# Kernel tuning notes

Measured on AMD Instinct MI355X. Metric: run time of the kernel, lower is better.

Reference implementation:

```python
import jax, jax.numpy as jnp
import numpy as np

KH, KW = 3, 3
STRIDE, PAD = 2, 1
NEG_SLOPE = 0.2
EPS = 1e-5


def conv2d(x, w, stride, pad):
    return jax.lax.conv_general_dilated(
        x, w, window_strides=(stride, stride),
        padding=[(pad, pad), (pad, pad)],
        dimension_numbers=('NCHW', 'OIHW', 'NCHW'))


def deform_conv2d(x, offsets, w_def):
    # x: [B,C,H,W]; offsets: [B,2*K,Ho,Wo] (per-kernel-tap (dy,dx) pairs);
    # w_def: [Cout,Cin,KH,KW]. Matches torchvision DeformConv2d (v1, no mask).
    B, C, H, W = x.shape
    Ho, Wo = offsets.shape[2], offsets.shape[3]
    K = KH * KW
    off = offsets.reshape(B, K, 2, Ho, Wo)
    dy, dx = off[:, :, 0], off[:, :, 1]            # [B,K,Ho,Wo]

    ky = jnp.arange(KH).repeat(KW).astype(x.dtype)   # [K]
    kx = jnp.tile(jnp.arange(KW), KH).astype(x.dtype)
    base_y = (jnp.arange(Ho) * STRIDE - PAD).astype(x.dtype)  # [Ho]
    base_x = (jnp.arange(Wo) * STRIDE - PAD).astype(x.dtype)

    # sampling positions [B,K,Ho,Wo]
    py = base_y[None, None, :, None] + ky[None, :, None, None] + dy
    px = base_x[None, None, None, :] + kx[None, :, None, None] + dx

    y0f = jnp.floor(py); x0f = jnp.floor(px)
    wy1 = py - y0f; wy0 = 1.0 - wy1
    wx1 = px - x0f; wx0 = 1.0 - wx1
    y0 = y0f.astype(jnp.int32); x0 = x0f.astype(jnp.int32)
    y1 = y0 + 1; x1 = x0 + 1

    xt = jnp.transpose(x, (0, 2, 3, 1))  # [B,H,W,C] for channel-last gather
    bidx = jnp.arange(B)[:, None, None, None]

    def corner(yi, xi):
        valid = ((yi >= 0) & (yi < H) & (xi >= 0) & (xi < W)).astype(x.dtype)
        yc = jnp.clip(yi, 0, H - 1); xc = jnp.clip(xi, 0, W - 1)
        v = xt[bidx, yc, xc]                         # [B,K,Ho,Wo,C]
        return v * valid[..., None]

    sampled = (corner(y0, x0) * (wy0 * wx0)[..., None]
               + corner(y0, x1) * (wy0 * wx1)[..., None]
               + corner(y1, x0) * (wy1 * wx0)[..., None]
               + corner(y1, x1) * (wy1 * wx1)[..., None])  # [B,K,Ho,Wo,C]

    wk = w_def.reshape(w_def.shape[0], w_def.shape[1], K)   # [Cout,Cin,K]
    return jnp.einsum('bkhwc,ock->bohw', sampled, wk)


def leaky_relu(x):
    return jnp.where(x >= 0, x, NEG_SLOPE * x)


def instance_norm(x):
    mean = jnp.mean(x, axis=(2, 3), keepdims=True)
    var = jnp.var(x, axis=(2, 3), keepdims=True)
    return (x - mean) * jax.lax.rsqrt(var + EPS)


def setup_inputs() -> dict:
    key = jax.random.key(0)
    k1, k2, k3, k4 = jax.random.split(key, 4)
    B, Cin, H, W = 8, 256, 128, 128
    Cout = 256
    x = jax.random.normal(k1, (B, Cin, H, W), dtype=jnp.float32)
    # conv_offset weight: predicts 2*K offset channels
    w_off = jax.random.normal(k2, (2 * KH * KW, Cin, KH, KW), dtype=jnp.float32) * 0.01
    w_def = jax.random.normal(k3, (Cout, Cin, KH, KW), dtype=jnp.float32) * 0.02
    w_1x1 = jax.random.normal(k4, (Cout, Cout, 1, 1), dtype=jnp.float32) * 0.02
    return {"x": x, "w_off": w_off, "w_def": w_def, "w_1x1": w_1x1}


def reference(x, w_off, w_def, w_1x1):
    offsets = conv2d(x, w_off, STRIDE, PAD)          # [B,18,Ho,Wo]
    y = deform_conv2d(x, offsets, w_def)             # [B,Cout,Ho,Wo]
    y = leaky_relu(y)
    y = conv2d(y, w_1x1, 1, 0)
    y = instance_norm(y)
    return leaky_relu(y)
```

## Files before the change

kernel.cpp:

```cpp
#include <hip/hip_runtime.h>

#define B_   8
#define CIN  256
#define H_   128
#define W_   128
#define HO   64
#define WO   64
#define CO_  256
#define NEG  0.2f

typedef __attribute__((ext_vector_type(8))) short bf16x8;
typedef __attribute__((ext_vector_type(4))) float f32x4;
typedef unsigned short u16;

#define OFF_OFS   0
#define WDEF_OFS  589824
#define W1_OFS    884736
#define WBOFF_OFS 917504
#define Y1_OFS    954368
#define XBF_OFS   5148672

__device__ __forceinline__ float lrelu(float v) { return v >= 0.f ? v : NEG * v; }

__device__ __forceinline__ u16 f2bf(float f) {
    unsigned u = __float_as_uint(f);
    u += 0x7FFFu + ((u >> 16) & 1u);
    return (u16)(u >> 16);
}
__device__ __forceinline__ float bf2f(u16 u) {
    return __uint_as_float(((unsigned)u) << 16);
}

__device__ __forceinline__ void gld16(const void* g, void* l) {
    __builtin_amdgcn_global_load_lds((const __attribute__((address_space(1))) unsigned*)g,
                                     (__attribute__((address_space(3))) unsigned*)l, 16, 0, 0);
}

__global__ __launch_bounds__(256) void prep(
    const float* __restrict__ wdef, const float* __restrict__ w1,
    const float* __restrict__ woff,
    u16* __restrict__ wdefbf, u16* __restrict__ w1bf, u16* __restrict__ wboff)
{
    int i = blockIdx.x * 256 + threadIdx.x;
    if (i < 9 * 256 * 256) {
        int c  = i & 255;
        int co = (i >> 8) & 255;
        int k  = i >> 16;
        wdefbf[i] = f2bf(wdef[((size_t)co * 256 + c) * 9 + k]);
    }
    if (i < 65536) w1bf[i] = f2bf(w1[i]);
    if (i < 73728) {
        int j  = i & 7;
        int s  = (i >> 3) & 7;
        int co = (i >> 6) & 31;
        int ch = (i >> 11) & 3;
        int k  = i >> 13;
        int c  = ch * 64 + ((s ^ ((co >> 1) & 7)) << 3) + j;
        wboff[i] = (co < 18) ? f2bf(woff[((size_t)co * 256 + c) * 9 + k]) : (u16)0;
    }
}

__global__ __launch_bounds__(256) void nchw2nhwc(
    const float* __restrict__ x, u16* __restrict__ xbf)
{
    __shared__ float tile[64][128];
    int bid = blockIdx.x;
    int g = bid & 3;
    int y = (bid >> 2) & 127;
    int b = bid >> 9;
    int t = threadIdx.x;

    const float* src = x + ((size_t)(b * 256 + g * 64) * 128 + y) * 128;
#pragma unroll
    for (int p = 0; p < 8; ++p) {
        int i = p * 256 + t;
        int cc = i >> 5, x4 = (i & 31) * 4;
        *(float4*)&tile[cc][x4] = *(const float4*)(src + (size_t)cc * 16384 + x4);
    }
    __syncthreads();

    int xpos = t >> 1, h = t & 1;
    u16 buf[32];
#pragma unroll
    for (int j = 0; j < 32; ++j) buf[j] = f2bf(tile[h * 32 + j][xpos]);
    u16* dst = xbf + (((size_t)b * 128 + y) * 128 + xpos) * 256 + g * 64 + h * 32;
#pragma unroll
    for (int q = 0; q < 4; ++q)
        *(int4*)(dst + q * 8) = *(int4*)(buf + q * 8);
}

__global__ __launch_bounds__(256) void offconv_mfma(
    const u16* __restrict__ xbf, const u16* __restrict__ wboff,
    float* __restrict__ off)
{
    __shared__ __align__(16) char smem[57728];
    u16* xrowU = (u16*)smem;
    u16* bU    = (u16*)(smem + 49536);

    int blk = blockIdx.x;
    blk = (blk & 7) * 64 + (blk >> 3);
    int b = blk >> 6, ho = blk & 63;
    int t = threadIdx.x;
    int lane = t & 63, w = t >> 6;
    int r = lane & 15, kg = lane >> 4;

    const u16* xB = xbf + (size_t)b * (128 * 128 * 256);

    f32x4 acc[2];
    acc[0] = f32x4{0.f, 0.f, 0.f, 0.f};
    acc[1] = f32x4{0.f, 0.f, 0.f, 0.f};

    if (t < 24) {
        int ry = t >> 3, s = t & 7;
        *(int4*)(smem + (ry * 129 * 8 + s) * 16) = int4{0, 0, 0, 0};
    }

    for (int ch = 0; ch < 4; ++ch) {
        __syncthreads();
        for (int ry = 0; ry < 3; ++ry) {
            int y = 2 * ho - 1 + ry;
            int rowbase = (ry * 129 + 1) * 128;
            if ((unsigned)y < 128u) {
#pragma unroll
                for (int p = 0; p < 4; ++p) {
                    int u = p * 256 + t;
                    int xpi = u >> 3, s = u & 7;
                    int c8 = s ^ (((xpi + 1) >> 1) & 7);
                    gld16(xB + ((size_t)(y * 128 + xpi)) * 256 + ch * 64 + c8 * 8,
                          smem + rowbase + p * 4096 + w * 1024);
                }
            } else if (ch == 0) {
#pragma unroll
                for (int p = 0; p < 4; ++p)
                    *(int4*)(smem + rowbase + (p * 256 + t) * 16) = int4{0, 0, 0, 0};
            }
        }
        gld16(wboff + (size_t)(0 * 4 + ch) * 2048 + t * 8,
              smem + 49536 + w * 1024);
        __syncthreads();

        for (int k = 0; k < 9; ++k) {
            int buf = k & 1;
            if (k < 8)
                gld16(wboff + (size_t)((k + 1) * 4 + ch) * 2048 + t * 8,
                      smem + 49536 + (buf ^ 1) * 4096 + w * 1024);
            int ky = k / 3, kx = k - 3 * ky;
            int pixA = w * 16 + r;
            int xp = 2 * pixA + kx;
            int abase = (ky * 129 + xp) * 64;
            int swA = (xp >> 1) & 7;
#pragma unroll
            for (int ksub = 0; ksub < 2; ++ksub) {
                int lc = ksub * 4 + kg;
                bf16x8 a = *(bf16x8*)(xrowU + abase + ((lc ^ swA) << 3));
#pragma unroll
                for (int n = 0; n < 2; ++n) {
                    int co = n * 16 + r;
                    bf16x8 bb = *(bf16x8*)(bU + buf * 2048 + co * 64 +
                                           ((lc ^ ((co >> 1) & 7)) << 3));
                    acc[n] = __builtin_amdgcn_mfma_f32_16x16x32_bf16(a, bb, acc[n], 0, 0, 0);
                }
            }
            __syncthreads();
        }
    }

#pragma unroll
    for (int n = 0; n < 2; ++n) {
        int co = n * 16 + r;
        if (co < 18) {
#pragma unroll
            for (int j = 0; j < 4; ++j) {
                int wo = w * 16 + kg * 4 + j;
                off[(((size_t)b * 18 + co) * 64 + ho) * 64 + wo] = acc[n][j];
            }
        }
    }
}

__global__ __launch_bounds__(512, 4) void deform_nhwc(
    const u16* __restrict__ xbf, const float* __restrict__ off,
    const u16* __restrict__ wdefbf, u16* __restrict__ y1p)
{
    extern __shared__ __align__(16) char smem[];

    int blk = blockIdx.x;
    blk = (blk & 7) * 64 + (blk >> 3);
    int b = blk >> 6, ho = blk & 63;
    int t = threadIdx.x;
    int lane = t & 63, w = t >> 6;
    int r = lane & 15, kg = lane >> 4;
    int pixS = w * 8 + (lane >> 3);
    int cs   = lane & 7;

    f32x4 acc[4][2];
    f32x4 zz = {0.f, 0.f, 0.f, 0.f};
#pragma unroll
    for (int m = 0; m < 4; ++m)
#pragma unroll
        for (int n = 0; n < 2; ++n) acc[m][n] = zz;

    const u16* xB = xbf + (size_t)b * (128 * 128 * 256);

    int o00, o01, o10, o11;
    float f00, f01, f10, f11;

    auto coords = [&](int k) {
        int ky = k / 3, kx = k - 3 * ky;
        float dy = off[(((size_t)b * 18 + 2 * k    ) * 64 + ho) * 64 + pixS];
        float dx = off[(((size_t)b * 18 + 2 * k + 1) * 64 + ho) * 64 + pixS];
        float py = (float)(ho * 2 - 1 + ky) + dy;
        float px = (float)(pixS * 2 - 1 + kx) + dx;
        float y0f = floorf(py), x0f = floorf(px);
        int y0 = (int)y0f, x0i = (int)x0f;
        float wy1 = py - y0f, wx1 = px - x0f;
        float wy0 = 1.f - wy1, wx0 = 1.f - wx1;
        int y1i = y0 + 1, x1i = x0i + 1;
        bool vy0 = (unsigned)y0  < 128u;
        bool vy1 = (unsigned)y1i < 128u;
        bool vx0 = (unsigned)x0i < 128u;
        bool vx1 = (unsigned)x1i < 128u;
        int yc0 = min(max(y0, 0), 127), yc1 = min(max(y1i, 0), 127);
        int xc0 = min(max(x0i, 0), 127), xc1 = min(max(x1i, 0), 127);
        o00 = yc0 * 128 + xc0;  o01 = yc0 * 128 + xc1;
        o10 = yc1 * 128 + xc0;  o11 = yc1 * 128 + xc1;
        f00 = (vy0 && vx0) ? wy0 * wx0 : 0.f;
        f01 = (vy0 && vx1) ? wy0 * wx1 : 0.f;
        f10 = (vy1 && vx0) ? wy1 * wx0 : 0.f;
        f11 = (vy1 && vx1) ? wy1 * wx1 : 0.f;
    };

    auto stage = [&](int k, int ch, int dbuf) {
        const u16* wk = wdefbf + ((size_t)k << 16);
#pragma unroll
        for (int p2 = 0; p2 < 4; ++p2) {
            int i = p2 * 512 + t;
            int co = i >> 3, s = i & 7;
            gld16(wk + (size_t)co * 256 + ch * 64 + ((s ^ (co & 7)) << 3),
                  smem + dbuf * 32768 + p2 * 8192 + w * 1024);
        }
    };

    auto sample = [&](int ch, int dbuf) {
        int cw = ch * 64 + cs * 8;
        const u16* q00 = xB + (size_t)o00 * 256 + cw;
        const u16* q01 = xB + (size_t)o01 * 256 + cw;
        const u16* q10 = xB + (size_t)o10 * 256 + cw;
        const u16* q11 = xB + (size_t)o11 * 256 + cw;
        bf16x8 c00 = *(const bf16x8*)q00;
        bf16x8 c01 = *(const bf16x8*)q01;
        bf16x8 c10 = *(const bf16x8*)q10;
        bf16x8 c11 = *(const bf16x8*)q11;
        u16 pk[8];
#pragma unroll
        for (int j = 0; j < 8; ++j) {
            float v = bf2f((u16)c00[j]) * f00 + bf2f((u16)c01[j]) * f01 +
                      bf2f((u16)c10[j]) * f10 + bf2f((u16)c11[j]) * f11;
            pk[j] = f2bf(v);
        }
        *(bf16x8*)(smem + 65536 + dbuf * 8192 + pixS * 128 + ((cs ^ (pixS & 7)) << 4)) =
            *(bf16x8*)pk;
    };

    coords(0);
    stage(0, 0, 0);
    sample(0, 0);
    __syncthreads();

    for (int p = 0; p < 36; ++p) {
        int cur = p & 1;
        if (p < 35) {
            int pn = p + 1;
            int chn = pn / 9, kn = pn - 9 * chn;
            stage(kn, chn, cur ^ 1);
            coords(kn);
            sample(chn, cur ^ 1);
        }
        u16* wb = (u16*)(smem + cur * 32768);
        u16* sb = (u16*)(smem + 65536 + cur * 8192);
        bf16x8 af[4], bfr[2];
        __builtin_amdgcn_s_setprio(1);
#pragma unroll
        for (int ksub = 0; ksub < 2; ++ksub) {
            int so = ((ksub * 4 + kg) ^ (r & 7)) << 3;
#pragma unroll
            for (int m = 0; m < 4; ++m)
                af[m] = *(bf16x8*)(sb + (m * 16 + r) * 64 + so);
#pragma unroll
            for (int n = 0; n < 2; ++n)
                bfr[n] = *(bf16x8*)(wb + (w * 32 + n * 16 + r) * 64 + so);
#pragma unroll
            for (int m = 0; m < 4; ++m)
#pragma unroll
                for (int n = 0; n < 2; ++n)
                    acc[m][n] = __builtin_amdgcn_mfma_f32_16x16x32_bf16(af[m], bfr[n], acc[m][n], 0, 0, 0);
        }
        __builtin_amdgcn_s_setprio(0);
        __syncthreads();
    }

    u16* outT = (u16*)smem;
    int rg = lane >> 4;
#pragma unroll
    for (int m = 0; m < 4; ++m)
#pragma unroll
        for (int n = 0; n < 2; ++n) {
            int co = w * 32 + n * 16 + r;
#pragma unroll
            for (int j = 0; j < 4; ++j) {
                int prow = m * 16 + rg * 4 + j;
                outT[prow * 256 + co] = f2bf(lrelu(acc[m][n][j]));
            }
        }
    __syncthreads();
    u16* dst = y1p + (size_t)(b * 64 + ho) * 16384;
#pragma unroll
    for (int p = 0; p < 4; ++p)
        *(int4*)((char*)dst + p * 8192 + t * 16) = *(int4*)(smem + p * 8192 + t * 16);
}

__global__ __launch_bounds__(256) void conv1x1_mfma(
    const u16* __restrict__ y1p, const u16* __restrict__ w1bf,
    float* __restrict__ out)
{
    __shared__ __align__(16) char smem[20480];
    u16* btile = (u16*)smem;
    u16* atile = (u16*)(smem + 16384);

    int blk = blockIdx.x;
    blk = (blk & 7) * 64 + (blk >> 3);
    int b = blk >> 6, ho = blk & 63;
    int t = threadIdx.x, lane = t & 63, w = t >> 6;
    int r = lane & 15, kg = lane >> 4;
    int sR = (r >> 1) & 3;

    f32x4 acc[4][4];
    f32x4 zz = {0.f, 0.f, 0.f, 0.f};
#pragma unroll
    for (int m = 0; m < 4; ++m)
#pragma unroll
        for (int n = 0; n < 4; ++n) acc[m][n] = zz;

    const u16* abase = y1p + (size_t)(b * 64 + ho) * 16384;

    for (int ch = 0; ch < 8; ++ch) {
#pragma unroll
        for (int p = 0; p < 4; ++p) {
            int slot = p * 256 + t;
            int o = slot >> 2, qq = slot & 3;
            gld16(w1bf + o * 256 + ch * 32 + ((qq ^ ((o >> 1) & 3)) << 3),
                  smem + p * 4096 + (t >> 6) * 1024);
        }
        {
            int pix = t >> 2, qq = t & 3;
            gld16(abase + pix * 256 + ch * 32 + ((qq ^ ((pix >> 1) & 3)) << 3),
                  smem + 16384 + (t >> 6) * 1024);
        }
        __syncthreads();
        bf16x8 af[4], bfr[4];
#pragma unroll
        for (int m = 0; m < 4; ++m)
            af[m] = *(bf16x8*)(atile + (m * 16 + r) * 32 + ((kg ^ sR) << 3));
#pragma unroll
        for (int n = 0; n < 4; ++n)
            bfr[n] = *(bf16x8*)(btile + (w * 64 + n * 16 + r) * 32 + ((kg ^ sR) << 3));
#pragma unroll
        for (int m = 0; m < 4; ++m)
#pragma unroll
            for (int n = 0; n < 4; ++n)
                acc[m][n] = __builtin_amdgcn_mfma_f32_16x16x32_bf16(af[m], bfr[n], acc[m][n], 0, 0, 0);
        __syncthreads();
    }

    int rg = lane >> 4;
#pragma unroll
    for (int m = 0; m < 4; ++m)
#pragma unroll
        for (int n = 0; n < 4; ++n) {
            int o = w * 64 + n * 16 + r;
            int pix0 = m * 16 + rg * 4;
            float4 v;
            v.x = acc[m][n][0]; v.y = acc[m][n][1];
            v.z = acc[m][n][2]; v.w = acc[m][n][3];
            *(float4*)(out + ((size_t)(b * 256 + o) * 64 + ho) * 64 + pix0) = v;
        }
}

__global__ __launch_bounds__(256) void instnorm(float* __restrict__ out)
{
    int bc = blockIdx.x;
    float* p = out + (size_t)bc * 4096;
    int t = threadIdx.x;

    float4 v[4];
    float s1 = 0.f, s2 = 0.f;
#pragma unroll
    for (int i = 0; i < 4; ++i) {
        v[i] = *(const float4*)&p[(t + i * 256) * 4];
        s1 += v[i].x + v[i].y + v[i].z + v[i].w;
        s2 += v[i].x * v[i].x + v[i].y * v[i].y + v[i].z * v[i].z + v[i].w * v[i].w;
    }
#pragma unroll
    for (int o = 32; o > 0; o >>= 1) {
        s1 += __shfl_down(s1, o);
        s2 += __shfl_down(s2, o);
    }
    __shared__ float rs[8];
    __shared__ float mb[2];
    int wave = t >> 6;
    if ((t & 63) == 0) { rs[wave] = s1; rs[4 + wave] = s2; }
    __syncthreads();
    if (t == 0) {
        float a = rs[0] + rs[1] + rs[2] + rs[3];
        float qq = rs[4] + rs[5] + rs[6] + rs[7];
        float mean = a * (1.f / 4096.f);
        float var  = qq * (1.f / 4096.f) - mean * mean;
        mb[0] = mean;
        mb[1] = rsqrtf(var + 1e-5f);
    }
    __syncthreads();
    float mean = mb[0], inv = mb[1];
#pragma unroll
    for (int i = 0; i < 4; ++i) {
        float4 u = v[i];
        u.x = lrelu((u.x - mean) * inv);
        u.y = lrelu((u.y - mean) * inv);
        u.z = lrelu((u.z - mean) * inv);
        u.w = lrelu((u.w - mean) * inv);
        *(float4*)&p[(t + i * 256) * 4] = u;
    }
}

extern "C" void kernel_launch(void* const* d_in, const int* in_sizes, int n_in,
                              void* d_out, int out_size, void* d_ws, size_t ws_size,
                              hipStream_t stream)
{
    const float* x     = (const float*)d_in[0];
    const float* w_off = (const float*)d_in[1];
    const float* w_def = (const float*)d_in[2];
    const float* w1    = (const float*)d_in[3];
    float* out = (float*)d_out;
    float* ws  = (float*)d_ws;

    float* off    = ws + OFF_OFS;
    u16*   wdefbf = (u16*)(ws + WDEF_OFS);
    u16*   w1bf   = (u16*)(ws + W1_OFS);
    u16*   wboff  = (u16*)(ws + WBOFF_OFS);
    u16*   y1p    = (u16*)(ws + Y1_OFS);
    u16*   xbf    = (u16*)(ws + XBF_OFS);

    hipFuncSetAttribute((const void*)deform_nhwc,
                        hipFuncAttributeMaxDynamicSharedMemorySize, 81920);

    hipLaunchKernelGGL(prep,         dim3(2304), dim3(256), 0, stream, w_def, w1, w_off, wdefbf, w1bf, wboff);
    hipLaunchKernelGGL(nchw2nhwc,    dim3(4096), dim3(256), 0, stream, x, xbf);
    hipLaunchKernelGGL(offconv_mfma, dim3(512),  dim3(256), 0, stream, xbf, wboff, off);
    hipLaunchKernelGGL(deform_nhwc,  dim3(512),  dim3(512), 81920, stream, xbf, off, wdefbf, y1p);
    hipLaunchKernelGGL(conv1x1_mfma, dim3(512),  dim3(256), 0, stream, y1p, w1bf, out);
    hipLaunchKernelGGL(instnorm,     dim3(2048), dim3(256), 0, stream, out);
}
```

Before: 164.2 us.

## Split offset conv over channel groups, load operands directly from global, add reduction

The offset convolution now splits the 256 input channels into four groups across 4x more blocks. Each block reads its A and B operands straight from global memory into registers instead of staging them in LDS behind barriers. A new reduce kernel sums the four partial outputs into the offset buffer. The partials reuse the y1 workspace region, which is safe only because the reduction finishes before deform writes y1. The change adds partial-sum traffic and an extra launch in exchange for more parallelism and no LDS synchronisation.

```diff
diff --git a/kernel.cpp b/kernel.cpp
--- a/kernel.cpp
+++ b/kernel.cpp
@@ -18,6 +18,7 @@
 #define W1_OFS    884736
 #define WBOFF_OFS 917504
 #define Y1_OFS    954368
+#define PART_OFS  954368
 #define XBF_OFS   5148672
 
 __device__ __forceinline__ float lrelu(float v) { return v >= 0.f ? v : NEG * v; }
@@ -39,7 +40,7 @@
 __global__ __launch_bounds__(256) void prep(
     const float* __restrict__ wdef, const float* __restrict__ w1,
     const float* __restrict__ woff,
-    u16* __restrict__ wdefbf, u16* __restrict__ w1bf, u16* __restrict__ wboff)
+    u16* __restrict__ wdefbf, u16* __restrict__ w1bf, u16* __restrict__ wboff2)
 {
     int i = blockIdx.x * 256 + threadIdx.x;
     if (i < 9 * 256 * 256) {
@@ -50,13 +51,12 @@
     }
     if (i < 65536) w1bf[i] = f2bf(w1[i]);
     if (i < 73728) {
-        int j  = i & 7;
-        int s  = (i >> 3) & 7;
+        int j  = i & 63;
         int co = (i >> 6) & 31;
-        int ch = (i >> 11) & 3;
+        int g  = (i >> 11) & 3;
         int k  = i >> 13;
-        int c  = ch * 64 + ((s ^ ((co >> 1) & 7)) << 3) + j;
-        wboff[i] = (co < 18) ? f2bf(woff[((size_t)co * 256 + c) * 9 + k]) : (u16)0;
+        int c  = g * 64 + j;
+        wboff2[i] = (co < 18) ? f2bf(woff[((size_t)co * 256 + c) * 9 + k]) : (u16)0;
     }
 }
 
@@ -89,18 +89,16 @@
         *(int4*)(dst + q * 8) = *(int4*)(buf + q * 8);
 }
 
-__global__ __launch_bounds__(256) void offconv_mfma(
-    const u16* __restrict__ xbf, const u16* __restrict__ wboff,
-    float* __restrict__ off)
-{
-    __shared__ __align__(16) char smem[57728];
-    u16* xrowU = (u16*)smem;
-    u16* bU    = (u16*)(smem + 49536);
-
-    int blk = blockIdx.x;
-    blk = (blk & 7) * 64 + (blk >> 3);
-    int b = blk >> 6, ho = blk & 63;
-    int t = threadIdx.x;
+__global__ __launch_bounds__(256) void offconv_reg(
+    const u16* __restrict__ xbf, const u16* __restrict__ wboff2,
+    float* __restrict__ part)
+{
+    int bid = blockIdx.x;
+    int swz = (bid & 7) * 256 + (bid >> 3);
+    int b  = swz >> 8;
+    int g  = (swz >> 6) & 3;
+    int ho = swz & 63;
+    int t  = threadIdx.x;
     int lane = t & 63, w = t >> 6;
     int r = lane & 15, kg = lane >> 4;
 
@@ -110,58 +108,26 @@
     acc[0] = f32x4{0.f, 0.f, 0.f, 0.f};
     acc[1] = f32x4{0.f, 0.f, 0.f, 0.f};
 
-    if (t < 24) {
-        int ry = t >> 3, s = t & 7;
-        *(int4*)(smem + (ry * 129 * 8 + s) * 16) = int4{0, 0, 0, 0};
-    }
-
-    for (int ch = 0; ch < 4; ++ch) {
-        __syncthreads();
-        for (int ry = 0; ry < 3; ++ry) {
-            int y = 2 * ho - 1 + ry;
-            int rowbase = (ry * 129 + 1) * 128;
-            if ((unsigned)y < 128u) {
-#pragma unroll
-                for (int p = 0; p < 4; ++p) {
-                    int u = p * 256 + t;
-                    int xpi = u >> 3, s = u & 7;
-                    int c8 = s ^ (((xpi + 1) >> 1) & 7);
-                    gld16(xB + ((size_t)(y * 128 + xpi)) * 256 + ch * 64 + c8 * 8,
-                          smem + rowbase + p * 4096 + w * 1024);
-                }
-            } else if (ch == 0) {
-#pragma unroll
-                for (int p = 0; p < 4; ++p)
-                    *(int4*)(smem + rowbase + (p * 256 + t) * 16) = int4{0, 0, 0, 0};
+    int pxg = w * 16 + r;
+
+#pragma unroll
+    for (int k = 0; k < 9; ++k) {
+        int ky = k / 3, kx = k - 3 * ky;
+        int y  = 2 * ho  - 1 + ky;
+        int xp = 2 * pxg - 1 + kx;
+        bool av = ((unsigned)y < 128u) && ((unsigned)xp < 128u);
+        int yc = min(max(y, 0), 127), xc = min(max(xp, 0), 127);
+        const u16* abase = xB + ((size_t)(yc * 128 + xc)) * 256 + g * 64 + kg * 8;
+        const u16* bbase = wboff2 + ((size_t)(k * 4 + g) * 32) * 64 + kg * 8;
+#pragma unroll
+        for (int ks = 0; ks < 2; ++ks) {
+            bf16x8 a = *(const bf16x8*)(abase + ks * 32);
+            if (!av) a = (bf16x8)(short)0;
+#pragma unroll
+            for (int n = 0; n < 2; ++n) {
+                bf16x8 bb = *(const bf16x8*)(bbase + (size_t)(n * 16 + r) * 64 + ks * 32);
+                acc[n] = __builtin_amdgcn_mfma_f32_16x16x32_bf16(a, bb, acc[n], 0, 0, 0);
             }
-        }
-        gld16(wboff + (size_t)(0 * 4 + ch) * 2048 + t * 8,
-              smem + 49536 + w * 1024);
-        __syncthreads();
-
-        for (int k = 0; k < 9; ++k) {
-            int buf = k & 1;
-            if (k < 8)
-                gld16(wboff + (size_t)((k + 1) * 4 + ch) * 2048 + t * 8,
-                      smem + 49536 + (buf ^ 1) * 4096 + w * 1024);
-            int ky = k / 3, kx = k - 3 * ky;
-            int pixA = w * 16 + r;
-            int xp = 2 * pixA + kx;
-            int abase = (ky * 129 + xp) * 64;
-            int swA = (xp >> 1) & 7;
-#pragma unroll
-            for (int ksub = 0; ksub < 2; ++ksub) {
-                int lc = ksub * 4 + kg;
-                bf16x8 a = *(bf16x8*)(xrowU + abase + ((lc ^ swA) << 3));
-#pragma unroll
-                for (int n = 0; n < 2; ++n) {
-                    int co = n * 16 + r;
-                    bf16x8 bb = *(bf16x8*)(bU + buf * 2048 + co * 64 +
-                                           ((lc ^ ((co >> 1) & 7)) << 3));
-                    acc[n] = __builtin_amdgcn_mfma_f32_16x16x32_bf16(a, bb, acc[n], 0, 0, 0);
-                }
-            }
-            __syncthreads();
         }
     }
 
@@ -172,10 +138,27 @@
 #pragma unroll
             for (int j = 0; j < 4; ++j) {
                 int wo = w * 16 + kg * 4 + j;
-                off[(((size_t)b * 18 + co) * 64 + ho) * 64 + wo] = acc[n][j];
+                part[(((size_t)(g * 8 + b) * 18 + co) * 64 + ho) * 64 + wo] = acc[n][j];
             }
         }
     }
+}
+
+__global__ __launch_bounds__(256) void reduce_off(
+    const float* __restrict__ part, float* __restrict__ off)
+{
+    int i4 = blockIdx.x * 256 + threadIdx.x;
+    if (i4 >= 147456) return;
+    float4 a = *(const float4*)&part[(size_t)i4 * 4];
+    float4 b = *(const float4*)&part[(size_t)i4 * 4 + 589824];
+    float4 c = *(const float4*)&part[(size_t)i4 * 4 + 2 * 589824];
+    float4 d = *(const float4*)&part[(size_t)i4 * 4 + 3 * 589824];
+    float4 o;
+    o.x = (a.x + b.x) + (c.x + d.x);
+    o.y = (a.y + b.y) + (c.y + d.y);
+    o.z = (a.z + b.z) + (c.z + d.z);
+    o.w = (a.w + b.w) + (c.w + d.w);
+    *(float4*)&off[(size_t)i4 * 4] = o;
 }
 
 __global__ __launch_bounds__(512, 4) void deform_nhwc(
@@ -445,16 +428,18 @@
     float* off    = ws + OFF_OFS;
     u16*   wdefbf = (u16*)(ws + WDEF_OFS);
     u16*   w1bf   = (u16*)(ws + W1_OFS);
-    u16*   wboff  = (u16*)(ws + WBOFF_OFS);
+    u16*   wboff2 = (u16*)(ws + WBOFF_OFS);
     u16*   y1p    = (u16*)(ws + Y1_OFS);
+    float* part   = ws + PART_OFS;
     u16*   xbf    = (u16*)(ws + XBF_OFS);
 
     hipFuncSetAttribute((const void*)deform_nhwc,
                         hipFuncAttributeMaxDynamicSharedMemorySize, 81920);
 
-    hipLaunchKernelGGL(prep,         dim3(2304), dim3(256), 0, stream, w_def, w1, w_off, wdefbf, w1bf, wboff);
+    hipLaunchKernelGGL(prep,         dim3(2304), dim3(256), 0, stream, w_def, w1, w_off, wdefbf, w1bf, wboff2);
     hipLaunchKernelGGL(nchw2nhwc,    dim3(4096), dim3(256), 0, stream, x, xbf);
-    hipLaunchKernelGGL(offconv_mfma, dim3(512),  dim3(256), 0, stream, xbf, wboff, off);
+    hipLaunchKernelGGL(offconv_reg,  dim3(2048), dim3(256), 0, stream, xbf, wboff2, part);
+    hipLaunchKernelGGL(reduce_off,   dim3(576),  dim3(256), 0, stream, part, off);
     hipLaunchKernelGGL(deform_nhwc,  dim3(512),  dim3(512), 81920, stream, xbf, off, wdefbf, y1p);
     hipLaunchKernelGGL(conv1x1_mfma, dim3(512),  dim3(256), 0, stream, y1p, w1bf, out);
     hipLaunchKernelGGL(instnorm,     dim3(2048), dim3(256), 0, stream, out);
```

Result: slower. 195.7 us (+19.2%).
